# Kernel optimization log

Measured on AMD Instinct MI355X. Metric: run time of the kernel, lower is better.

The kernel has to match this reference:

```python
import jax, jax.numpy as jnp
import numpy as np

N = 100000
E = 3200000
NEG_SLOPE = 0.2  # PyG GATConv default


def gat_layer(x, src, dst, W, a_src, a_dst, b, heads, out_ch, concat):
    # per-node linear transform, split into heads: [N, H, C]
    h = (x @ W).reshape(N, heads, out_ch)
    # per-node attention logits: [N, H]
    al_src = jnp.sum(h * a_src, axis=-1)
    al_dst = jnp.sum(h * a_dst, axis=-1)
    # per-edge attention coefficient (x_j = source, x_i = target): [E, H]
    e = jax.nn.leaky_relu(al_src[src] + al_dst[dst], NEG_SLOPE)
    # segment softmax over incoming edges of each destination node
    m = jax.ops.segment_max(e, dst, num_segments=N)
    e = jnp.exp(e - m[dst])
    denom = jax.ops.segment_sum(e, dst, num_segments=N)
    alpha = e / (denom[dst] + 1e-16)
    # weighted message aggregation: scatter-add over dst
    msg = h[src] * alpha[..., None]  # [E, H, C]
    out = jax.ops.segment_sum(msg, dst, num_segments=N)  # [N, H, C]
    out = out.reshape(N, heads * out_ch) if concat else out.mean(axis=1)
    return out + b


def setup_inputs() -> dict:
    key = jax.random.key(0)
    ks = jax.random.split(key, 11)
    return {
        "x": jax.random.normal(ks[0], (N, 2), dtype=jnp.float32),
        "edge_index": jax.random.randint(ks[1], (2, E), 0, N, dtype=jnp.int64),
        "edge_attr": jax.random.normal(ks[2], (E, 1), dtype=jnp.float32),
        "W1": jax.random.normal(ks[3], (2, 32), dtype=jnp.float32) * 0.5,
        "att_src1": jax.random.normal(ks[4], (4, 8), dtype=jnp.float32) * 0.3,
        "att_dst1": jax.random.normal(ks[5], (4, 8), dtype=jnp.float32) * 0.3,
        "b1": jnp.zeros((32,), dtype=jnp.float32),
        "W2": jax.random.normal(ks[6], (32, 2), dtype=jnp.float32) * 0.2,
        "att_src2": jax.random.normal(ks[7], (1, 2), dtype=jnp.float32) * 0.3,
        "att_dst2": jax.random.normal(ks[8], (1, 2), dtype=jnp.float32) * 0.3,
        "b2": jnp.zeros((2,), dtype=jnp.float32),
    }


def reference(x, edge_index, edge_attr, W1, att_src1, att_dst1, b1, W2, att_src2, att_dst2, b2):
    # add self-loops (PyG GATConv default add_self_loops=True)
    loops = jnp.arange(N, dtype=edge_index.dtype)
    src = jnp.concatenate([edge_index[0], loops])
    dst = jnp.concatenate([edge_index[1], loops])
    h = gat_layer(x, src, dst, W1, att_src1, att_dst1, b1, heads=4, out_ch=8, concat=True)
    h = jax.nn.elu(h)
    out = gat_layer(h, src, dst, W2, att_src2, att_dst2, b2, heads=1, out_ch=2, concat=False)
    return out
```

## Files before the change

### kernel.cpp

```cpp
#include <hip/hip_runtime.h>
#include <hip/hip_bf16.h>
#include <math.h>

#define NEG_SLOPE 0.2f
#define BK_BITS 9
#define BK (1 << BK_BITS)
#define SBITS 17
#define SMASK ((1 << SBITS) - 1)
#define CAP 20480
#define RSTRIDE (CAP + 4 * BK)
#define PPT 17

__device__ __forceinline__ float lrelu(float x) { return x > 0.f ? x : NEG_SLOPE * x; }

__global__ void init_bcur(int* __restrict__ bcur, int NB) {
    int i = threadIdx.x;
    if (i < NB) bcur[i] = i * CAP;
}

__global__ __launch_bounds__(256) void bucket_scatter(const int* __restrict__ src,
                                                      const int* __restrict__ dst,
                                                      int* __restrict__ bcur,
                                                      int* __restrict__ pairs, int E) {
    __shared__ int cnt[256], sc[256], off[256], cur[256], gbase[256];
    __shared__ int lpair[4096];
    __shared__ unsigned char lbkt[4096];
    int t = threadIdx.x;
    cnt[t] = 0;
    __syncthreads();

    int E4 = E >> 2;
    const int4* src4 = (const int4*)src;
    const int4* dst4 = (const int4*)dst;
    int base4 = blockIdx.x * 1024;
    int4 d4[4], s4[4];
    bool val[4];
#pragma unroll
    for (int k = 0; k < 4; k++) {
        int i4 = base4 + k * 256 + t;
        val[k] = (i4 < E4);
        if (val[k]) {
            d4[k] = dst4[i4];
            s4[k] = src4[i4];
            atomicAdd(&cnt[d4[k].x >> BK_BITS], 1);
            atomicAdd(&cnt[d4[k].y >> BK_BITS], 1);
            atomicAdd(&cnt[d4[k].z >> BK_BITS], 1);
            atomicAdd(&cnt[d4[k].w >> BK_BITS], 1);
        }
    }
    int dt = -1, st = 0;
    if (blockIdx.x == gridDim.x - 1) {
        int e = (E4 << 2) + t;
        if (e < E) { dt = dst[e]; st = src[e]; atomicAdd(&cnt[dt >> BK_BITS], 1); }
    }
    __syncthreads();

    sc[t] = cnt[t];
    __syncthreads();
    for (int o = 1; o < 256; o <<= 1) {
        int u = (t >= o) ? sc[t - o] : 0;
        __syncthreads();
        sc[t] += u;
        __syncthreads();
    }
    int excl = (t == 0) ? 0 : sc[t - 1];
    off[t] = excl;
    cur[t] = excl;
    if (cnt[t] > 0) gbase[t] = atomicAdd(&bcur[t], cnt[t]);
    __syncthreads();
    int total = sc[255];

#pragma unroll
    for (int k = 0; k < 4; k++) {
        if (val[k]) {
            int b, slot;
            b = d4[k].x >> BK_BITS; slot = atomicAdd(&cur[b], 1);
            lpair[slot] = ((d4[k].x & (BK - 1)) << SBITS) | s4[k].x; lbkt[slot] = (unsigned char)b;
            b = d4[k].y >> BK_BITS; slot = atomicAdd(&cur[b], 1);
            lpair[slot] = ((d4[k].y & (BK - 1)) << SBITS) | s4[k].y; lbkt[slot] = (unsigned char)b;
            b = d4[k].z >> BK_BITS; slot = atomicAdd(&cur[b], 1);
            lpair[slot] = ((d4[k].z & (BK - 1)) << SBITS) | s4[k].z; lbkt[slot] = (unsigned char)b;
            b = d4[k].w >> BK_BITS; slot = atomicAdd(&cur[b], 1);
            lpair[slot] = ((d4[k].w & (BK - 1)) << SBITS) | s4[k].w; lbkt[slot] = (unsigned char)b;
        }
    }
    if (dt >= 0) {
        int b = dt >> BK_BITS;
        int slot = atomicAdd(&cur[b], 1);
        lpair[slot] = ((dt & (BK - 1)) << SBITS) | st; lbkt[slot] = (unsigned char)b;
    }
    __syncthreads();

    for (int i = t; i < total; i += 256) {
        int b = lbkt[i];
        pairs[gbase[b] + (i - off[b])] = lpair[i];
    }
}

__global__ __launch_bounds__(1024) void csr_build(const int* __restrict__ pairs,
                                                  const int* __restrict__ bcur,
                                                  int* __restrict__ row_deg,
                                                  int* __restrict__ csr_src, int N) {
    int b = blockIdx.x;
    int t = threadIdx.x;
    int lo = b * CAP, hi = bcur[b];
    int dbase = b << BK_BITS;
    int ndst = min(BK, N - dbase);
    int base2 = b * RSTRIDE;
    __shared__ int cnt[BK];
    __shared__ int sc[256];
    __shared__ int cur[BK];
    if (t < BK) cnt[t] = 0;
    __syncthreads();

    int myp[PPT];
#pragma unroll
    for (int k = 0; k < PPT; k++) {
        int i = lo + t + k * 1024;
        int p = (i < hi) ? pairs[i] : -1;
        myp[k] = p;
        if (p >= 0) atomicAdd(&cnt[p >> SBITS], 1);
    }
    for (int i = lo + t + PPT * 1024; i < hi; i += 1024)
        atomicAdd(&cnt[pairs[i] >> SBITS], 1);
    __syncthreads();

    int d0 = 0, d1 = 0, a0 = 0, a1 = 0;
    if (t < 256) {
        int i0 = 2 * t, i1 = 2 * t + 1;
        d0 = (i0 < ndst) ? cnt[i0] + 1 : 0;
        d1 = (i1 < ndst) ? cnt[i1] + 1 : 0;
        a0 = (d0 + 3) & ~3;
        a1 = (d1 + 3) & ~3;
        sc[t] = a0 + a1;
    }
    __syncthreads();
    for (int o = 1; o < 256; o <<= 1) {
        int u = 0;
        if (t < 256 && t >= o) u = sc[t - o];
        __syncthreads();
        if (t < 256) sc[t] += u;
        __syncthreads();
    }
    if (t < 256) {
        int excl = (t == 0) ? 0 : sc[t - 1];
        int i0 = 2 * t, i1 = 2 * t + 1;
        if (i0 < ndst) {
            row_deg[dbase + i0] = (excl << 16) | d0;
            csr_src[base2 + excl] = dbase + i0;
            for (int k = d0; k < a0; k++) csr_src[base2 + excl + k] = dbase + i0;
            cur[i0] = excl + 1;
        }
        excl += a0;
        if (i1 < ndst) {
            row_deg[dbase + i1] = (excl << 16) | d1;
            csr_src[base2 + excl] = dbase + i1;
            for (int k = d1; k < a1; k++) csr_src[base2 + excl + k] = dbase + i1;
            cur[i1] = excl + 1;
        }
    }
    __syncthreads();

#pragma unroll
    for (int k = 0; k < PPT; k++) {
        int p = myp[k];
        if (p >= 0) {
            int pos = atomicAdd(&cur[p >> SBITS], 1);
            csr_src[base2 + pos] = p & SMASK;
        }
    }
    for (int i = lo + t + PPT * 1024; i < hi; i += 1024) {
        int p = pairs[i];
        int pos = atomicAdd(&cur[p >> SBITS], 1);
        csr_src[base2 + pos] = p & SMASK;
    }
}

__global__ __launch_bounds__(256) void agg1_dstlane(
        const int* __restrict__ row_deg, const int* __restrict__ csr_src,
        const float2* __restrict__ x2,
        const float* __restrict__ W1, const float* __restrict__ asrc,
        const float* __restrict__ adst, const float* __restrict__ b1,
        const float* __restrict__ W2, const float* __restrict__ as2,
        const float* __restrict__ ad2,
        float2* __restrict__ h2, float* __restrict__ al2d, int N) {
    __shared__ float sW[64], sB[32], sW2[64], sP[4], sQ[4], sPd[4], sQd[4], sA2[4];
    int t = threadIdx.x;
    if (t < 64) { sW[t] = W1[t]; sW2[t] = W2[t]; }
    if (t < 32) sB[t] = b1[t];
    if (t < 2) { sA2[t] = as2[t]; sA2[2 + t] = ad2[t]; }
    if (t < 4) {
        float P = 0.f, Q = 0.f, Pd = 0.f, Qd = 0.f;
#pragma unroll
        for (int k = 0; k < 8; k++) {
            int c = t * 8 + k;
            float a = asrc[c], ad_ = adst[c];
            float w0 = W1[c], w1 = W1[32 + c];
            P += w0 * a; Q += w1 * a;
            Pd += w0 * ad_; Qd += w1 * ad_;
        }
        sP[t] = P; sQ[t] = Q; sPd[t] = Pd; sQd[t] = Qd;
    }
    __syncthreads();

    int tid = blockIdx.x * blockDim.x + t;
    int n = tid >> 2;
    int q = tid & 3;
    if (n >= N) return;
    int rd = row_deg[n];
    int row = (n >> BK_BITS) * RSTRIDE + (rd >> 16);
    int deg = rd & 0xFFFF;

    float2 xd = x2[n];
    float P[4], Q[4], ald[4];
#pragma unroll
    for (int h = 0; h < 4; h++) {
        P[h] = sP[h]; Q[h] = sQ[h];
        ald[h] = xd.x * sPd[h] + xd.y * sQd[h];
    }

    float Sw[4] = {0.f, 0.f, 0.f, 0.f};
    float S0[4] = {0.f, 0.f, 0.f, 0.f};
    float S1[4] = {0.f, 0.f, 0.f, 0.f};
    for (int j = q * 4; j < deg; j += 16) {
        int4 s4 = *(const int4*)(csr_src + row + j);
        float2 xs[4];
        xs[0] = x2[s4.x]; xs[1] = x2[s4.y]; xs[2] = x2[s4.z]; xs[3] = x2[s4.w];
#pragma unroll
        for (int k = 0; k < 4; k++) {
            bool live = (j + k < deg);
#pragma unroll
            for (int h = 0; h < 4; h++) {
                float e = lrelu(fmaf(xs[k].x, P[h], fmaf(xs[k].y, Q[h], ald[h])));
                float w = __expf(fminf(e, 80.f));
                w = live ? w : 0.f;
                Sw[h] += w;
                S0[h] += w * xs[k].x;
                S1[h] += w * xs[k].y;
            }
        }
    }
#pragma unroll
    for (int o = 1; o <= 2; o <<= 1) {
#pragma unroll
        for (int h = 0; h < 4; h++) {
            Sw[h] += __shfl_xor(Sw[h], o);
            S0[h] += __shfl_xor(S0[h], o);
            S1[h] += __shfl_xor(S1[h], o);
        }
    }
    if (q != 0) return;

    float r[4];
#pragma unroll
    for (int h = 0; h < 4; h++) r[h] = 1.f / (Sw[h] + 1e-16f);
    float h20 = 0.f, h21 = 0.f;
#pragma unroll
    for (int c = 0; c < 32; c++) {
        int h = c >> 3;
        float outc = (sW[c] * S0[h] + sW[32 + c] * S1[h]) * r[h];
        float v2 = outc + sB[c];
        v2 = v2 > 0.f ? v2 : __expf(v2) - 1.f;
        h20 = fmaf(v2, sW2[2 * c], h20);
        h21 = fmaf(v2, sW2[2 * c + 1], h21);
    }
    h2[n] = make_float2(h20, h21);
    al2d[n] = h20 * sA2[2] + h21 * sA2[3];
}

__global__ __launch_bounds__(256) void agg2_dstlane(
        const int* __restrict__ row_deg, const int* __restrict__ csr_src,
        const float* __restrict__ al2d, const float2* __restrict__ h2,
        const float* __restrict__ as2, const float* __restrict__ b2,
        float2* __restrict__ out, int N) {
    int tid = blockIdx.x * blockDim.x + threadIdx.x;
    int n = tid >> 2;
    int q = tid & 3;
    if (n >= N) return;
    int rd = row_deg[n];
    int row = (n >> BK_BITS) * RSTRIDE + (rd >> 16);
    int deg = rd & 0xFFFF;
    float ald = al2d[n];
    float a0 = as2[0], a1 = as2[1];

    float wsum = 0.f, ax = 0.f, ay = 0.f;
    for (int j = q * 4; j < deg; j += 16) {
        int4 s4 = *(const int4*)(csr_src + row + j);
        float2 hv[4];
        hv[0] = h2[s4.x]; hv[1] = h2[s4.y]; hv[2] = h2[s4.z]; hv[3] = h2[s4.w];
#pragma unroll
        for (int k = 0; k < 4; k++) {
            float e = lrelu(fmaf(hv[k].x, a0, fmaf(hv[k].y, a1, ald)));
            float w = __expf(fminf(e, 80.f));
            w = (j + k < deg) ? w : 0.f;
            wsum += w;
            ax = fmaf(w, hv[k].x, ax);
            ay = fmaf(w, hv[k].y, ay);
        }
    }
#pragma unroll
    for (int o = 1; o <= 2; o <<= 1) {
        wsum += __shfl_xor(wsum, o);
        ax += __shfl_xor(ax, o);
        ay += __shfl_xor(ay, o);
    }
    if (q != 0) return;
    float inv = 1.f / (wsum + 1e-16f);
    out[n] = make_float2(ax * inv + b2[0], ay * inv + b2[1]);
}

extern "C" void kernel_launch(void* const* d_in, const int* in_sizes, int n_in,
                              void* d_out, int out_size, void* d_ws, size_t ws_size,
                              hipStream_t stream) {
    const float* x     = (const float*)d_in[0];
    const int*   eidx  = (const int*)d_in[1];
    const float* W1    = (const float*)d_in[3];
    const float* asrc1 = (const float*)d_in[4];
    const float* adst1 = (const float*)d_in[5];
    const float* b1    = (const float*)d_in[6];
    const float* W2    = (const float*)d_in[7];
    const float* asrc2 = (const float*)d_in[8];
    const float* adst2 = (const float*)d_in[9];
    const float* b2    = (const float*)d_in[10];

    const int N = in_sizes[0] / 2;
    const int E = in_sizes[1] / 2;
    const int* src = eidx;
    const int* dst = eidx + E;
    const int NB = (N + BK - 1) >> BK_BITS;

    float* w = (float*)d_ws;
    float2* h2    = (float2*)w;
    float*  al2d  = w + 2 * (size_t)N;
    int* ip       = (int*)(w + 3 * (size_t)N);
    int* row_deg  = ip;
    int* bcur     = ip + (size_t)N;
    int* pairs    = ip + (size_t)N + NB;
    int* csr_src  = pairs + (size_t)NB * CAP;

    const int B = 256;
    int E4 = E >> 2;
    int gS = (E4 + 1023) / 1024;
    int gL4 = (4 * N + B - 1) / B;

    init_bcur<<<1, B, 0, stream>>>(bcur, NB);
    bucket_scatter<<<gS, B, 0, stream>>>(src, dst, bcur, pairs, E);
    csr_build<<<NB, 1024, 0, stream>>>(pairs, bcur, row_deg, csr_src, N);

    agg1_dstlane<<<gL4, B, 0, stream>>>(row_deg, csr_src, (const float2*)x,
                                        W1, asrc1, adst1, b1, W2, asrc2, adst2,
                                        h2, al2d, N);
    agg2_dstlane<<<gL4, B, 0, stream>>>(row_deg, csr_src, al2d, h2, asrc2, b2,
                                        (float2*)d_out, N);
}
```

Measured before the change: 184.9 us.

## Drop CSR build and aggregate directly from dst buckets with LDS atomics

```diff
diff --git a/kernel.cpp b/kernel.cpp
--- a/kernel.cpp
+++ b/kernel.cpp
@@ -1,5 +1,4 @@
 #include <hip/hip_runtime.h>
-#include <hip/hip_bf16.h>
 #include <math.h>
 
 #define NEG_SLOPE 0.2f
@@ -8,8 +7,6 @@
 #define SBITS 17
 #define SMASK ((1 << SBITS) - 1)
 #define CAP 20480
-#define RSTRIDE (CAP + 4 * BK)
-#define PPT 17
 
 __device__ __forceinline__ float lrelu(float x) { return x > 0.f ? x : NEG_SLOPE * x; }
 
@@ -97,87 +94,8 @@
     }
 }
 
-__global__ __launch_bounds__(1024) void csr_build(const int* __restrict__ pairs,
-                                                  const int* __restrict__ bcur,
-                                                  int* __restrict__ row_deg,
-                                                  int* __restrict__ csr_src, int N) {
-    int b = blockIdx.x;
-    int t = threadIdx.x;
-    int lo = b * CAP, hi = bcur[b];
-    int dbase = b << BK_BITS;
-    int ndst = min(BK, N - dbase);
-    int base2 = b * RSTRIDE;
-    __shared__ int cnt[BK];
-    __shared__ int sc[256];
-    __shared__ int cur[BK];
-    if (t < BK) cnt[t] = 0;
-    __syncthreads();
-
-    int myp[PPT];
-#pragma unroll
-    for (int k = 0; k < PPT; k++) {
-        int i = lo + t + k * 1024;
-        int p = (i < hi) ? pairs[i] : -1;
-        myp[k] = p;
-        if (p >= 0) atomicAdd(&cnt[p >> SBITS], 1);
-    }
-    for (int i = lo + t + PPT * 1024; i < hi; i += 1024)
-        atomicAdd(&cnt[pairs[i] >> SBITS], 1);
-    __syncthreads();
-
-    int d0 = 0, d1 = 0, a0 = 0, a1 = 0;
-    if (t < 256) {
-        int i0 = 2 * t, i1 = 2 * t + 1;
-        d0 = (i0 < ndst) ? cnt[i0] + 1 : 0;
-        d1 = (i1 < ndst) ? cnt[i1] + 1 : 0;
-        a0 = (d0 + 3) & ~3;
-        a1 = (d1 + 3) & ~3;
-        sc[t] = a0 + a1;
-    }
-    __syncthreads();
-    for (int o = 1; o < 256; o <<= 1) {
-        int u = 0;
-        if (t < 256 && t >= o) u = sc[t - o];
-        __syncthreads();
-        if (t < 256) sc[t] += u;
-        __syncthreads();
-    }
-    if (t < 256) {
-        int excl = (t == 0) ? 0 : sc[t - 1];
-        int i0 = 2 * t, i1 = 2 * t + 1;
-        if (i0 < ndst) {
-            row_deg[dbase + i0] = (excl << 16) | d0;
-            csr_src[base2 + excl] = dbase + i0;
-            for (int k = d0; k < a0; k++) csr_src[base2 + excl + k] = dbase + i0;
-            cur[i0] = excl + 1;
-        }
-        excl += a0;
-        if (i1 < ndst) {
-            row_deg[dbase + i1] = (excl << 16) | d1;
-            csr_src[base2 + excl] = dbase + i1;
-            for (int k = d1; k < a1; k++) csr_src[base2 + excl + k] = dbase + i1;
-            cur[i1] = excl + 1;
-        }
-    }
-    __syncthreads();
-
-#pragma unroll
-    for (int k = 0; k < PPT; k++) {
-        int p = myp[k];
-        if (p >= 0) {
-            int pos = atomicAdd(&cur[p >> SBITS], 1);
-            csr_src[base2 + pos] = p & SMASK;
-        }
-    }
-    for (int i = lo + t + PPT * 1024; i < hi; i += 1024) {
-        int p = pairs[i];
-        int pos = atomicAdd(&cur[p >> SBITS], 1);
-        csr_src[base2 + pos] = p & SMASK;
-    }
-}
-
-__global__ __launch_bounds__(256) void agg1_dstlane(
-        const int* __restrict__ row_deg, const int* __restrict__ csr_src,
+__global__ __launch_bounds__(1024) void agg1_bucket(
+        const int* __restrict__ pairs, const int* __restrict__ bcur,
         const float2* __restrict__ x2,
         const float* __restrict__ W1, const float* __restrict__ asrc,
         const float* __restrict__ adst, const float* __restrict__ b1,
@@ -185,7 +103,10 @@
         const float* __restrict__ ad2,
         float2* __restrict__ h2, float* __restrict__ al2d, int N) {
     __shared__ float sW[64], sB[32], sW2[64], sP[4], sQ[4], sPd[4], sQd[4], sA2[4];
+    __shared__ float4 sAld[BK];
+    __shared__ float sAcc[12 * BK];
     int t = threadIdx.x;
+    int b = blockIdx.x;
     if (t < 64) { sW[t] = W1[t]; sW2[t] = W2[t]; }
     if (t < 32) sB[t] = b1[t];
     if (t < 2) { sA2[t] = as2[t]; sA2[2 + t] = ad2[t]; }
@@ -203,110 +124,139 @@
     }
     __syncthreads();
 
-    int tid = blockIdx.x * blockDim.x + t;
-    int n = tid >> 2;
-    int q = tid & 3;
-    if (n >= N) return;
-    int rd = row_deg[n];
-    int row = (n >> BK_BITS) * RSTRIDE + (rd >> 16);
-    int deg = rd & 0xFFFF;
-
-    float2 xd = x2[n];
-    float P[4], Q[4], ald[4];
-#pragma unroll
-    for (int h = 0; h < 4; h++) {
-        P[h] = sP[h]; Q[h] = sQ[h];
-        ald[h] = xd.x * sPd[h] + xd.y * sQd[h];
-    }
-
-    float Sw[4] = {0.f, 0.f, 0.f, 0.f};
-    float S0[4] = {0.f, 0.f, 0.f, 0.f};
-    float S1[4] = {0.f, 0.f, 0.f, 0.f};
-    for (int j = q * 4; j < deg; j += 16) {
-        int4 s4 = *(const int4*)(csr_src + row + j);
+    float rP[4], rQ[4];
+#pragma unroll
+    for (int h = 0; h < 4; h++) { rP[h] = sP[h]; rQ[h] = sQ[h]; }
+
+    int dbase = b << BK_BITS;
+    int ndst = min(BK, N - dbase);
+
+    if (t < ndst) {
+        float2 xd = x2[dbase + t];
+        float ald[4];
+#pragma unroll
+        for (int h = 0; h < 4; h++) {
+            ald[h] = xd.x * sPd[h] + xd.y * sQd[h];
+            float e = lrelu(fmaf(xd.x, rP[h], fmaf(xd.y, rQ[h], ald[h])));
+            float w = __expf(fminf(e, 80.f));
+            sAcc[h * BK + t] = w;
+            sAcc[4 * BK + h * BK + t] = w * xd.x;
+            sAcc[8 * BK + h * BK + t] = w * xd.y;
+        }
+        sAld[t] = make_float4(ald[0], ald[1], ald[2], ald[3]);
+    }
+    __syncthreads();
+
+    int lo = b * CAP, hi = bcur[b];
+    for (int base = lo + (t << 2); base < hi; base += 4096) {
+        int4 p4 = *(const int4*)(pairs + base);
+        int pv[4] = {p4.x, p4.y, p4.z, p4.w};
+        int nlive = min(hi - base, 4);
         float2 xs[4];
-        xs[0] = x2[s4.x]; xs[1] = x2[s4.y]; xs[2] = x2[s4.z]; xs[3] = x2[s4.w];
 #pragma unroll
         for (int k = 0; k < 4; k++) {
-            bool live = (j + k < deg);
-#pragma unroll
-            for (int h = 0; h < 4; h++) {
-                float e = lrelu(fmaf(xs[k].x, P[h], fmaf(xs[k].y, Q[h], ald[h])));
-                float w = __expf(fminf(e, 80.f));
-                w = live ? w : 0.f;
-                Sw[h] += w;
-                S0[h] += w * xs[k].x;
-                S1[h] += w * xs[k].y;
+            int s = (k < nlive) ? (pv[k] & SMASK) : 0;
+            xs[k] = x2[s];
+        }
+#pragma unroll
+        for (int k = 0; k < 4; k++) {
+            if (k < nlive) {
+                int dl = pv[k] >> SBITS;
+                float4 av = sAld[dl];
+                float alh[4] = {av.x, av.y, av.z, av.w};
+#pragma unroll
+                for (int h = 0; h < 4; h++) {
+                    float e = lrelu(fmaf(xs[k].x, rP[h], fmaf(xs[k].y, rQ[h], alh[h])));
+                    float w = __expf(fminf(e, 80.f));
+                    unsafeAtomicAdd(&sAcc[h * BK + dl], w);
+                    unsafeAtomicAdd(&sAcc[4 * BK + h * BK + dl], w * xs[k].x);
+                    unsafeAtomicAdd(&sAcc[8 * BK + h * BK + dl], w * xs[k].y);
+                }
             }
         }
     }
-#pragma unroll
-    for (int o = 1; o <= 2; o <<= 1) {
+    __syncthreads();
+
+    if (t < ndst) {
+        float r[4], S0[4], S1[4];
 #pragma unroll
         for (int h = 0; h < 4; h++) {
-            Sw[h] += __shfl_xor(Sw[h], o);
-            S0[h] += __shfl_xor(S0[h], o);
-            S1[h] += __shfl_xor(S1[h], o);
-        }
-    }
-    if (q != 0) return;
-
-    float r[4];
-#pragma unroll
-    for (int h = 0; h < 4; h++) r[h] = 1.f / (Sw[h] + 1e-16f);
-    float h20 = 0.f, h21 = 0.f;
-#pragma unroll
-    for (int c = 0; c < 32; c++) {
-        int h = c >> 3;
-        float outc = (sW[c] * S0[h] + sW[32 + c] * S1[h]) * r[h];
-        float v2 = outc + sB[c];
-        v2 = v2 > 0.f ? v2 : __expf(v2) - 1.f;
-        h20 = fmaf(v2, sW2[2 * c], h20);
-        h21 = fmaf(v2, sW2[2 * c + 1], h21);
-    }
-    h2[n] = make_float2(h20, h21);
-    al2d[n] = h20 * sA2[2] + h21 * sA2[3];
-}
-
-__global__ __launch_bounds__(256) void agg2_dstlane(
-        const int* __restrict__ row_deg, const int* __restrict__ csr_src,
-        const float* __restrict__ al2d, const float2* __restrict__ h2,
+            float sw = sAcc[h * BK + t];
+            r[h] = 1.f / (sw + 1e-16f);
+            S0[h] = sAcc[4 * BK + h * BK + t];
+            S1[h] = sAcc[8 * BK + h * BK + t];
+        }
+        float h20 = 0.f, h21 = 0.f;
+#pragma unroll
+        for (int c = 0; c < 32; c++) {
+            int h = c >> 3;
+            float outc = (sW[c] * S0[h] + sW[32 + c] * S1[h]) * r[h];
+            float v2 = outc + sB[c];
+            v2 = v2 > 0.f ? v2 : __expf(v2) - 1.f;
+            h20 = fmaf(v2, sW2[2 * c], h20);
+            h21 = fmaf(v2, sW2[2 * c + 1], h21);
+        }
+        int n = dbase + t;
+        h2[n] = make_float2(h20, h21);
+        al2d[n] = h20 * sA2[2] + h21 * sA2[3];
+    }
+}
+
+__global__ __launch_bounds__(1024) void agg2_bucket(
+        const int* __restrict__ pairs, const int* __restrict__ bcur,
+        const float2* __restrict__ h2, const float* __restrict__ al2d,
         const float* __restrict__ as2, const float* __restrict__ b2,
         float2* __restrict__ out, int N) {
-    int tid = blockIdx.x * blockDim.x + threadIdx.x;
-    int n = tid >> 2;
-    int q = tid & 3;
-    if (n >= N) return;
-    int rd = row_deg[n];
-    int row = (n >> BK_BITS) * RSTRIDE + (rd >> 16);
-    int deg = rd & 0xFFFF;
-    float ald = al2d[n];
+    __shared__ float sAld2[BK];
+    __shared__ float sAcc[3 * BK];
+    int t = threadIdx.x;
+    int b = blockIdx.x;
+    int dbase = b << BK_BITS;
+    int ndst = min(BK, N - dbase);
     float a0 = as2[0], a1 = as2[1];
 
-    float wsum = 0.f, ax = 0.f, ay = 0.f;
-    for (int j = q * 4; j < deg; j += 16) {
-        int4 s4 = *(const int4*)(csr_src + row + j);
+    if (t < ndst) {
+        float2 hv = h2[dbase + t];
+        float ald = al2d[dbase + t];
+        sAld2[t] = ald;
+        float e = lrelu(fmaf(hv.x, a0, fmaf(hv.y, a1, ald)));
+        float w = __expf(fminf(e, 80.f));
+        sAcc[t] = w;
+        sAcc[BK + t] = w * hv.x;
+        sAcc[2 * BK + t] = w * hv.y;
+    }
+    __syncthreads();
+
+    int lo = b * CAP, hi = bcur[b];
+    for (int base = lo + (t << 2); base < hi; base += 4096) {
+        int4 p4 = *(const int4*)(pairs + base);
+        int pv[4] = {p4.x, p4.y, p4.z, p4.w};
+        int nlive = min(hi - base, 4);
         float2 hv[4];
-        hv[0] = h2[s4.x]; hv[1] = h2[s4.y]; hv[2] = h2[s4.z]; hv[3] = h2[s4.w];
 #pragma unroll
         for (int k = 0; k < 4; k++) {
-            float e = lrelu(fmaf(hv[k].x, a0, fmaf(hv[k].y, a1, ald)));
-            float w = __expf(fminf(e, 80.f));
-            w = (j + k < deg) ? w : 0.f;
-            wsum += w;
-            ax = fmaf(w, hv[k].x, ax);
-            ay = fmaf(w, hv[k].y, ay);
-        }
-    }
-#pragma unroll
-    for (int o = 1; o <= 2; o <<= 1) {
-        wsum += __shfl_xor(wsum, o);
-        ax += __shfl_xor(ax, o);
-        ay += __shfl_xor(ay, o);
-    }
-    if (q != 0) return;
-    float inv = 1.f / (wsum + 1e-16f);
-    out[n] = make_float2(ax * inv + b2[0], ay * inv + b2[1]);
+            int s = (k < nlive) ? (pv[k] & SMASK) : 0;
+            hv[k] = h2[s];
+        }
+#pragma unroll
+        for (int k = 0; k < 4; k++) {
+            if (k < nlive) {
+                int dl = pv[k] >> SBITS;
+                float e = lrelu(fmaf(hv[k].x, a0, fmaf(hv[k].y, a1, sAld2[dl])));
+                float w = __expf(fminf(e, 80.f));
+                unsafeAtomicAdd(&sAcc[dl], w);
+                unsafeAtomicAdd(&sAcc[BK + dl], w * hv[k].x);
+                unsafeAtomicAdd(&sAcc[2 * BK + dl], w * hv[k].y);
+            }
+        }
+    }
+    __syncthreads();
+
+    if (t < ndst) {
+        float inv = 1.f / (sAcc[t] + 1e-16f);
+        out[dbase + t] = make_float2(sAcc[BK + t] * inv + b2[0],
+                                     sAcc[2 * BK + t] * inv + b2[1]);
+    }
 }
 
 extern "C" void kernel_launch(void* const* d_in, const int* in_sizes, int n_in,
@@ -333,23 +283,18 @@
     float2* h2    = (float2*)w;
     float*  al2d  = w + 2 * (size_t)N;
     int* ip       = (int*)(w + 3 * (size_t)N);
-    int* row_deg  = ip;
-    int* bcur     = ip + (size_t)N;
-    int* pairs    = ip + (size_t)N + NB;
-    int* csr_src  = pairs + (size_t)NB * CAP;
+    int* bcur     = ip;
+    int* pairs    = ip + 256;
 
     const int B = 256;
     int E4 = E >> 2;
     int gS = (E4 + 1023) / 1024;
-    int gL4 = (4 * N + B - 1) / B;
 
     init_bcur<<<1, B, 0, stream>>>(bcur, NB);
     bucket_scatter<<<gS, B, 0, stream>>>(src, dst, bcur, pairs, E);
-    csr_build<<<NB, 1024, 0, stream>>>(pairs, bcur, row_deg, csr_src, N);
-
-    agg1_dstlane<<<gL4, B, 0, stream>>>(row_deg, csr_src, (const float2*)x,
-                                        W1, asrc1, adst1, b1, W2, asrc2, adst2,
-                                        h2, al2d, N);
-    agg2_dstlane<<<gL4, B, 0, stream>>>(row_deg, csr_src, al2d, h2, asrc2, b2,
-                                        (float2*)d_out, N);
-}
+    agg1_bucket<<<NB, 1024, 0, stream>>>(pairs, bcur, (const float2*)x,
+                                         W1, asrc1, adst1, b1, W2, asrc2, adst2,
+                                         h2, al2d, N);
+    agg2_bucket<<<NB, 1024, 0, stream>>>(pairs, bcur, (const float2*)h2, al2d,
+                                         asrc2, b2, (float2*)d_out, N);
+}
```

Measured after the change: 448.8 us. +142.7%, slower.
